# Performance work log

Hardware: AMD Instinct MI355X
Metric: run time of the kernel (lower is better)

Reference implementation:

```python
import jax, jax.numpy as jnp
import numpy as np

FEATURE_BITWIDTH = 8
INPUT_ZERO_POINT = 0
OUTPUT_ZERO_POINT = 0
INPUT_SCALE = 0.02
OUTPUT_SCALE = 0.1
STRIDE = (1, 1)
PAD = (1, 1)  # (padH, padW)
DILATION = (1, 1)

QMIN = -(1 << (FEATURE_BITWIDTH - 1))          # -128
QMAX = (1 << (FEATURE_BITWIDTH - 1)) - 1       # 127


def setup_inputs() -> dict:
    key = jax.random.key(0)
    k1, k2, k3, k4 = jax.random.split(key, 4)
    N, Cin, H, W = 32, 128, 56, 56
    Cout, kH, kW = 256, 3, 3
    x = jax.random.randint(k1, (N, Cin, H, W), -128, 128, dtype=jnp.int32).astype(jnp.int8)
    weight = jax.random.randint(k2, (Cout, Cin, kH, kW), -128, 128, dtype=jnp.int32).astype(jnp.int8)
    bias = jax.random.randint(k3, (Cout,), -1000, 1000, dtype=jnp.int32)
    weight_scale = jax.random.uniform(k4, (Cout,), dtype=jnp.float32, minval=0.001, maxval=0.01)
    return {"x": x, "weight": weight, "bias": bias, "weight_scale": weight_scale}


def reference(x, weight, bias, weight_scale):
    # Pad spatial dims with the input zero point (asymmetric quant padding).
    padH, padW = PAD
    xp = jnp.pad(x.astype(jnp.int32),
                 ((0, 0), (0, 0), (padH, padH), (padW, padW)),
                 constant_values=INPUT_ZERO_POINT)
    # Integer conv accumulation in int32 (matches CPU path exactly).
    acc = jax.lax.conv_general_dilated(
        xp, weight.astype(jnp.int32),
        window_strides=STRIDE, padding='VALID',
        rhs_dilation=DILATION,
        dimension_numbers=('NCHW', 'OIHW', 'NCHW'))  # [N, Cout, Ho, Wo] int32
    acc = acc + bias[None, :, None, None]
    # Fused dequant -> requant epilogue with per-output-channel scale.
    scale = (INPUT_SCALE * weight_scale / OUTPUT_SCALE)[None, :, None, None]
    out = acc.astype(jnp.float32) * scale + OUTPUT_ZERO_POINT
    out = jnp.clip(jnp.round(out), QMIN, QMAX).astype(jnp.int8)
    return out
```

## Files before the change

kernel.cpp:

```cpp
#include <hip/hip_runtime.h>

#define N_      32
#define CIN     128
#define HW_     56
#define COUT    256
#define HP      58
#define SP_     (HW_*HW_)
#define M_      (N_*SP_)
#define ROWB    7424
#define CHB     928
#define XP_BYTES (N_*HP*ROWB)
#define WP_BYTES (9*COUT*CIN)

typedef int int4v  __attribute__((ext_vector_type(4)));
typedef int int16v __attribute__((ext_vector_type(16)));

__global__ __launch_bounds__(256) void repack_x(const int* __restrict__ x32,
                                                char* __restrict__ xp) {
    __shared__ char s8[CIN * HW_];
    int b = blockIdx.x;
    int n = b / HP;
    int hp = b - n * HP;
    int h = hp - 1;
    bool live = (h >= 0) && (h < HW_);
    if (live) {
        const int* src = x32 + ((size_t)(n * CIN)) * SP_ + h * HW_;
        for (int i = threadIdx.x; i < CIN * HW_; i += 256) {
            int c = i / HW_, w = i - c * HW_;
            s8[i] = (char)src[c * SP_ + w];
        }
    }
    __syncthreads();
    int* dst = (int*)(xp + (size_t)b * ROWB);
    for (int i = threadIdx.x; i < 8 * 232; i += 256) {
        int chunk = i / 232, r = i - chunk * 232;
        int wp = r >> 2, sub = r & 3;
        int w = wp - 1;
        int v = 0;
        if (live && w >= 0 && w < HW_) {
            int c0 = chunk * 16 + sub * 4;
            int v0 = (unsigned char)s8[(c0 + 0) * HW_ + w];
            int v1 = (unsigned char)s8[(c0 + 1) * HW_ + w];
            int v2 = (unsigned char)s8[(c0 + 2) * HW_ + w];
            int v3 = (unsigned char)s8[(c0 + 3) * HW_ + w];
            v = v0 | (v1 << 8) | (v2 << 16) | (v3 << 24);
        }
        dst[i] = v;
    }
}

__global__ __launch_bounds__(256) void repack_w(const int* __restrict__ w32,
                                                char* __restrict__ wp) {
    int i = blockIdx.x * 256 + threadIdx.x;
    int tap = i >> 13;
    int r   = i & 8191;
    int co  = r >> 5;
    int c4  = r & 31;
    const int* s = w32 + (co * CIN + c4 * 4) * 9 + tap;
    int v0 = s[0]  & 0xff;
    int v1 = s[9]  & 0xff;
    int v2 = s[18] & 0xff;
    int v3 = s[27] & 0xff;
    ((int*)wp)[i] = v0 | (v1 << 8) | (v2 << 16) | (v3 << 24);
}

__global__ __launch_bounds__(256, 2) void conv_mfma(const char* __restrict__ xp,
                                                    const char* __restrict__ wp,
                                                    const int*  __restrict__ bias,
                                                    const float* __restrict__ wsc,
                                                    int* __restrict__ out) {
    __shared__ char Bs[6 * 8192];
    const int tid  = threadIdx.x;
    const int wave = tid >> 6, lane = tid & 63;
    const int l31 = lane & 31, lh = lane >> 5;
    const int m_base = blockIdx.x << 8;
    const int co0    = blockIdx.y << 6;

    const char* aptrT[2];
    int tb[2];
#pragma unroll
    for (int mf = 0; mf < 2; ++mf) {
        tb[mf] = m_base + wave * 64 + mf * 32;
        int row = tb[mf] + l31;
        int n  = row / SP_;
        int sp = row - n * SP_;
        int ho = sp / HW_;
        int wo = sp - ho * HW_;
        aptrT[mf] = xp + (size_t)(n * HP + ho) * ROWB + lh * CHB + wo * 16;
    }

    const char* wpb = wp + co0 * CIN;

    int16v acc[2][2] = {};

    auto stageB = [&](int t0, int nt) {
        for (int i = wave; i < nt * 8; i += 4) {
            int p = (i << 10) + (lane << 4);
            int q = p ^ (((p >> 7) & 7) << 4);
            const char* src = wpb + (t0 + (p >> 13)) * (COUT * CIN) + (q & 8191);
            __builtin_amdgcn_global_load_lds(
                (const __attribute__((address_space(1))) void*)src,
                (__attribute__((address_space(3))) void*)&Bs[i << 10], 16, 0, 0);
        }
    };

    auto aload = [&](int4v a[2][4], int tap) {
        int kh = tap / 3, kw = tap - kh * 3;
        int aoff = kh * ROWB + kw * 16;
#pragma unroll
        for (int kc = 0; kc < 4; ++kc) {
            a[0][kc] = *(const int4v*)(aptrT[0] + aoff + kc * (2 * CHB));
            a[1][kc] = *(const int4v*)(aptrT[1] + aoff + kc * (2 * CHB));
        }
    };

    auto ctap = [&](const int4v a[2][4], int slab) {
        int bbase = slab << 13;
        int sw = (l31 & 7) << 4;
        int4v b0[4], b1[4];
#pragma unroll
        for (int kc = 0; kc < 4; ++kc) {
            int koff = kc * 32 + (lh << 4);
            b0[kc] = *(const int4v*)&Bs[(bbase + (l31 << 7) + koff) ^ sw];
            b1[kc] = *(const int4v*)&Bs[(bbase + ((l31 + 32) << 7) + koff) ^ sw];
        }
#pragma unroll
        for (int kc = 0; kc < 4; ++kc) {
            acc[0][0] = __builtin_amdgcn_mfma_i32_32x32x32_i8(a[0][kc], b0[kc], acc[0][0], 0, 0, 0);
            acc[1][0] = __builtin_amdgcn_mfma_i32_32x32x32_i8(a[1][kc], b0[kc], acc[1][0], 0, 0, 0);
            acc[0][1] = __builtin_amdgcn_mfma_i32_32x32x32_i8(a[0][kc], b1[kc], acc[0][1], 0, 0, 0);
            acc[1][1] = __builtin_amdgcn_mfma_i32_32x32x32_i8(a[1][kc], b1[kc], acc[1][1], 0, 0, 0);
        }
    };

    int4v aA[2][4], aB[2][4];

    stageB(0, 6);
    aload(aA, 0);
    __syncthreads();

    aload(aB, 1); ctap(aA, 0);
    aload(aA, 2); ctap(aB, 1);
    aload(aB, 3); ctap(aA, 2);
    __syncthreads();
    stageB(6, 3);
    aload(aA, 4); ctap(aB, 3);
    aload(aB, 5); ctap(aA, 4);
    aload(aA, 6); ctap(aB, 5);
    __syncthreads();
    aload(aB, 7); ctap(aA, 0);
    aload(aA, 8); ctap(aB, 1);
    ctap(aA, 2);

#pragma unroll
    for (int mf = 0; mf < 2; ++mf) {
        int nu  = tb[mf] / SP_;
        int sp0 = tb[mf] - nu * SP_;
#pragma unroll
        for (int nf = 0; nf < 2; ++nf) {
            int co = co0 + nf * 32 + l31;
            float s = (0.02f * wsc[co]) / 0.1f;
            int bs = bias[co];
            int* ob = out + ((size_t)(nu * COUT + co)) * SP_ + sp0 + (lh << 2);
#pragma unroll
            for (int g = 0; g < 4; ++g) {
                int4v qv;
#pragma unroll
                for (int r = 0; r < 4; ++r) {
                    float v = (float)(acc[mf][nf][g * 4 + r] + bs) * s;
                    int q = (int)rintf(v);
                    qv[r] = q < -128 ? -128 : (q > 127 ? 127 : q);
                }
                *(int4v*)(ob + g * 8) = qv;
            }
        }
    }
}

extern "C" void kernel_launch(void* const* d_in, const int* in_sizes, int n_in,
                              void* d_out, int out_size, void* d_ws, size_t ws_size,
                              hipStream_t stream) {
    const int*   x32  = (const int*)d_in[0];
    const int*   w32  = (const int*)d_in[1];
    const int*   bias = (const int*)d_in[2];
    const float* wsc  = (const float*)d_in[3];

    char* xp = (char*)d_ws;
    char* wp = xp + XP_BYTES;

    repack_x<<<dim3(N_ * HP), 256, 0, stream>>>(x32, xp);
    repack_w<<<dim3(WP_BYTES / 4 / 256), 256, 0, stream>>>(w32, wp);
    conv_mfma<<<dim3(M_ / 256, COUT / 64), 256, 0, stream>>>(xp, wp, bias, wsc,
                                                             (int*)d_out);
}
```

Measured before the change: 76.50 us.

## Widen Cout tile to 128 with double-buffered per-tap weight staging

Each block now computes 128 output channels instead of 64, so every A fragment loaded from global memory feeds twice as many MFMAs and the padded input is read half as often. Weight staging becomes a ping-pong of two 2-tap slabs in 64 KB of LDS, prefetching the next taps while the current ones are computed. MFMA sections are also wrapped in s_setprio. The cost is doubled accumulator registers (128 VGPRs for acc) and larger LDS, which may lower occupancy under the 2-block launch bound and halves the grid size.

```diff
diff --git a/kernel.cpp b/kernel.cpp
--- a/kernel.cpp
+++ b/kernel.cpp
@@ -11,6 +11,8 @@
 #define CHB     928
 #define XP_BYTES (N_*HP*ROWB)
 #define WP_BYTES (9*COUT*CIN)
+#define TAPB    (COUT*CIN)
+#define SLABB   16384
 
 typedef int int4v  __attribute__((ext_vector_type(4)));
 typedef int int16v __attribute__((ext_vector_type(16)));
@@ -69,12 +71,12 @@
                                                     const int*  __restrict__ bias,
                                                     const float* __restrict__ wsc,
                                                     int* __restrict__ out) {
-    __shared__ char Bs[6 * 8192];
+    __shared__ char Bs[4 * SLABB];
     const int tid  = threadIdx.x;
     const int wave = tid >> 6, lane = tid & 63;
     const int l31 = lane & 31, lh = lane >> 5;
     const int m_base = blockIdx.x << 8;
-    const int co0    = blockIdx.y << 6;
+    const int co0    = blockIdx.y << 7;
 
     const char* aptrT[2];
     int tb[2];
@@ -91,16 +93,16 @@
 
     const char* wpb = wp + co0 * CIN;
 
-    int16v acc[2][2] = {};
+    int16v acc[2][4] = {};
 
-    auto stageB = [&](int t0, int nt) {
-        for (int i = wave; i < nt * 8; i += 4) {
+    auto stageB = [&](int t0, int nt, int dst0) {
+        for (int i = wave; i < nt * 16; i += 4) {
             int p = (i << 10) + (lane << 4);
-            int q = p ^ (((p >> 7) & 7) << 4);
-            const char* src = wpb + (t0 + (p >> 13)) * (COUT * CIN) + (q & 8191);
+            int q = (p & (SLABB - 1)) ^ (((p >> 7) & 7) << 4);
+            const char* src = wpb + (t0 + (p >> 14)) * TAPB + q;
             __builtin_amdgcn_global_load_lds(
                 (const __attribute__((address_space(1))) void*)src,
-                (__attribute__((address_space(3))) void*)&Bs[i << 10], 16, 0, 0);
+                (__attribute__((address_space(3))) void*)&Bs[dst0 + (i << 10)], 16, 0, 0);
         }
     };
 
@@ -114,50 +116,52 @@
         }
     };
 
-    auto ctap = [&](const int4v a[2][4], int slab) {
-        int bbase = slab << 13;
-        int sw = (l31 & 7) << 4;
-        int4v b0[4], b1[4];
+    auto ctap = [&](const int4v a[2][4], int sbase) {
+        __builtin_amdgcn_s_setprio(1);
 #pragma unroll
-        for (int kc = 0; kc < 4; ++kc) {
-            int koff = kc * 32 + (lh << 4);
-            b0[kc] = *(const int4v*)&Bs[(bbase + (l31 << 7) + koff) ^ sw];
-            b1[kc] = *(const int4v*)&Bs[(bbase + ((l31 + 32) << 7) + koff) ^ sw];
+        for (int nf = 0; nf < 4; ++nf) {
+            int row0 = nf * 32 + l31;
+            int baddr = sbase + (row0 << 7) + (lh << 4);
+            int sw = (l31 & 7) << 4;
+            int4v b[4];
+#pragma unroll
+            for (int kc = 0; kc < 4; ++kc)
+                b[kc] = *(const int4v*)&Bs[(baddr + kc * 32) ^ sw];
+#pragma unroll
+            for (int kc = 0; kc < 4; ++kc) {
+                acc[0][nf] = __builtin_amdgcn_mfma_i32_32x32x32_i8(a[0][kc], b[kc], acc[0][nf], 0, 0, 0);
+                acc[1][nf] = __builtin_amdgcn_mfma_i32_32x32x32_i8(a[1][kc], b[kc], acc[1][nf], 0, 0, 0);
+            }
         }
-#pragma unroll
-        for (int kc = 0; kc < 4; ++kc) {
-            acc[0][0] = __builtin_amdgcn_mfma_i32_32x32x32_i8(a[0][kc], b0[kc], acc[0][0], 0, 0, 0);
-            acc[1][0] = __builtin_amdgcn_mfma_i32_32x32x32_i8(a[1][kc], b0[kc], acc[1][0], 0, 0, 0);
-            acc[0][1] = __builtin_amdgcn_mfma_i32_32x32x32_i8(a[0][kc], b1[kc], acc[0][1], 0, 0, 0);
-            acc[1][1] = __builtin_amdgcn_mfma_i32_32x32x32_i8(a[1][kc], b1[kc], acc[1][1], 0, 0, 0);
-        }
+        __builtin_amdgcn_s_setprio(0);
     };
 
     int4v aA[2][4], aB[2][4];
 
-    stageB(0, 6);
+    stageB(0, 2, 0);
     aload(aA, 0);
     __syncthreads();
 
-    aload(aB, 1); ctap(aA, 0);
-    aload(aA, 2); ctap(aB, 1);
-    aload(aB, 3); ctap(aA, 2);
+    stageB(2, 2, 32768); aload(aB, 1); ctap(aA, 0);
+    aload(aA, 2);                      ctap(aB, SLABB);
     __syncthreads();
-    stageB(6, 3);
-    aload(aA, 4); ctap(aB, 3);
-    aload(aB, 5); ctap(aA, 4);
-    aload(aA, 6); ctap(aB, 5);
+    stageB(4, 2, 0);     aload(aB, 3); ctap(aA, 32768);
+    aload(aA, 4);                      ctap(aB, 49152);
     __syncthreads();
-    aload(aB, 7); ctap(aA, 0);
-    aload(aA, 8); ctap(aB, 1);
-    ctap(aA, 2);
+    stageB(6, 2, 32768); aload(aB, 5); ctap(aA, 0);
+    aload(aA, 6);                      ctap(aB, SLABB);
+    __syncthreads();
+    stageB(8, 1, 0);     aload(aB, 7); ctap(aA, 32768);
+    aload(aA, 8);                      ctap(aB, 49152);
+    __syncthreads();
+    ctap(aA, 0);
 
 #pragma unroll
     for (int mf = 0; mf < 2; ++mf) {
         int nu  = tb[mf] / SP_;
         int sp0 = tb[mf] - nu * SP_;
 #pragma unroll
-        for (int nf = 0; nf < 2; ++nf) {
+        for (int nf = 0; nf < 4; ++nf) {
             int co = co0 + nf * 32 + l31;
             float s = (0.02f * wsc[co]) / 0.1f;
             int bs = bias[co];
@@ -190,6 +194,6 @@
 
     repack_x<<<dim3(N_ * HP), 256, 0, stream>>>(x32, xp);
     repack_w<<<dim3(WP_BYTES / 4 / 256), 256, 0, stream>>>(w32, wp);
-    conv_mfma<<<dim3(M_ / 256, COUT / 64), 256, 0, stream>>>(xp, wp, bias, wsc,
-                                                             (int*)d_out);
+    conv_mfma<<<dim3(M_ / 256, COUT / 128), 256, 0, stream>>>(xp, wp, bias, wsc,
+                                                              (int*)d_out);
 }
```

New measurement: 103.3 us. 1.35x slower.

## Remap workgroups XCD-aware, raise occupancy to 3 waves, prioritize MFMA sections

Applied to the files above, without the earlier changes.

The conv grid is flattened to 1D and block IDs are remapped so that consecutive logical tiles, with the four Cout tiles sharing an M tile adjacent, land on the same XCD. This is meant to improve L2 reuse of the repacked input across the output-channel tiles. Launch bounds rise from 2 to 3 blocks per CU to add latency hiding, at the risk of register pressure or spills. The MFMA section is also wrapped in s_setprio to favor compute waves, and the stageB indexing is slightly refactored.

```diff
diff --git a/kernel.cpp b/kernel.cpp
--- a/kernel.cpp
+++ b/kernel.cpp
@@ -11,6 +11,9 @@
 #define CHB     928
 #define XP_BYTES (N_*HP*ROWB)
 #define WP_BYTES (9*COUT*CIN)
+#define TAPB    (COUT*CIN)
+#define NWG     ((M_/256)*(COUT/64))
+#define PERX    (NWG/8)
 
 typedef int int4v  __attribute__((ext_vector_type(4)));
 typedef int int16v __attribute__((ext_vector_type(16)));
@@ -64,7 +67,7 @@
     ((int*)wp)[i] = v0 | (v1 << 8) | (v2 << 16) | (v3 << 24);
 }
 
-__global__ __launch_bounds__(256, 2) void conv_mfma(const char* __restrict__ xp,
+__global__ __launch_bounds__(256, 3) void conv_mfma(const char* __restrict__ xp,
                                                     const char* __restrict__ wp,
                                                     const int*  __restrict__ bias,
                                                     const float* __restrict__ wsc,
@@ -73,8 +76,11 @@
     const int tid  = threadIdx.x;
     const int wave = tid >> 6, lane = tid & 63;
     const int l31 = lane & 31, lh = lane >> 5;
-    const int m_base = blockIdx.x << 8;
-    const int co0    = blockIdx.y << 6;
+
+    int bid = blockIdx.x;
+    int w_  = (bid & 7) * PERX + (bid >> 3);
+    const int co0    = (w_ & 3) << 6;
+    const int m_base = (w_ >> 2) << 8;
 
     const char* aptrT[2];
     int tb[2];
@@ -93,14 +99,15 @@
 
     int16v acc[2][2] = {};
 
-    auto stageB = [&](int t0, int nt) {
+    auto stageB = [&](int t0, int nt, int slab0) {
         for (int i = wave; i < nt * 8; i += 4) {
             int p = (i << 10) + (lane << 4);
-            int q = p ^ (((p >> 7) & 7) << 4);
-            const char* src = wpb + (t0 + (p >> 13)) * (COUT * CIN) + (q & 8191);
+            int q = (p & 8191) ^ (((p >> 7) & 7) << 4);
+            const char* src = wpb + (t0 + (p >> 13)) * TAPB + q;
             __builtin_amdgcn_global_load_lds(
                 (const __attribute__((address_space(1))) void*)src,
-                (__attribute__((address_space(3))) void*)&Bs[i << 10], 16, 0, 0);
+                (__attribute__((address_space(3))) void*)&Bs[(slab0 << 13) + (i << 10)],
+                16, 0, 0);
         }
     };
 
@@ -114,15 +121,17 @@
         }
     };
 
+    const int sw = (l31 & 7) << 4;
+
     auto ctap = [&](const int4v a[2][4], int slab) {
         int bbase = slab << 13;
-        int sw = (l31 & 7) << 4;
+        __builtin_amdgcn_s_setprio(1);
         int4v b0[4], b1[4];
 #pragma unroll
         for (int kc = 0; kc < 4; ++kc) {
-            int koff = kc * 32 + (lh << 4);
-            b0[kc] = *(const int4v*)&Bs[(bbase + (l31 << 7) + koff) ^ sw];
-            b1[kc] = *(const int4v*)&Bs[(bbase + ((l31 + 32) << 7) + koff) ^ sw];
+            int koff = bbase + kc * 32 + (lh << 4);
+            b0[kc] = *(const int4v*)&Bs[(koff + (l31 << 7)) ^ sw];
+            b1[kc] = *(const int4v*)&Bs[(koff + ((l31 + 32) << 7)) ^ sw];
         }
 #pragma unroll
         for (int kc = 0; kc < 4; ++kc) {
@@ -131,11 +140,12 @@
             acc[0][1] = __builtin_amdgcn_mfma_i32_32x32x32_i8(a[0][kc], b1[kc], acc[0][1], 0, 0, 0);
             acc[1][1] = __builtin_amdgcn_mfma_i32_32x32x32_i8(a[1][kc], b1[kc], acc[1][1], 0, 0, 0);
         }
+        __builtin_amdgcn_s_setprio(0);
     };
 
     int4v aA[2][4], aB[2][4];
 
-    stageB(0, 6);
+    stageB(0, 6, 0);
     aload(aA, 0);
     __syncthreads();
 
@@ -143,7 +153,7 @@
     aload(aA, 2); ctap(aB, 1);
     aload(aB, 3); ctap(aA, 2);
     __syncthreads();
-    stageB(6, 3);
+    stageB(6, 3, 0);
     aload(aA, 4); ctap(aB, 3);
     aload(aB, 5); ctap(aA, 4);
     aload(aA, 6); ctap(aB, 5);
@@ -190,6 +200,5 @@
 
     repack_x<<<dim3(N_ * HP), 256, 0, stream>>>(x32, xp);
     repack_w<<<dim3(WP_BYTES / 4 / 256), 256, 0, stream>>>(w32, wp);
-    conv_mfma<<<dim3(M_ / 256, COUT / 64), 256, 0, stream>>>(xp, wp, bias, wsc,
-                                                             (int*)d_out);
-}
+    conv_mfma<<<dim3(NWG), 256, 0, stream>>>(xp, wp, bias, wsc, (int*)d_out);
+}
```

New measurement: 111.6 us. 1.46x slower.
